# Optimization experiments

Hardware: AMD Instinct MI355X
Metric: run time of the kernel (lower is better)

The kernel has to match this reference:

```python
import jax, jax.numpy as jnp
import numpy as np

B, S, F, E, C = 8, 8192, 512, 128, 1000


def setup_inputs() -> dict:
    key = jax.random.key(0)
    k1, k2, k3, k4 = jax.random.split(key, 4)
    x = jax.random.normal(k1, (B, F), dtype=jnp.float32)
    support_x = jax.random.normal(k2, (B, S, F), dtype=jnp.float32)
    support_y = jax.random.uniform(k3, (B, S, C), dtype=jnp.float32)
    # xavier_uniform on (1, F, E): gain * sqrt(6/(fan_in+fan_out))
    limit = float(np.sqrt(6.0 / (F + E)))
    proj_weight = jax.random.uniform(k4, (1, F, E), dtype=jnp.float32,
                                     minval=-limit, maxval=limit)
    return {"x": x, "support_x": support_x, "support_y": support_y,
            "proj_weight": proj_weight}


def reference(x, support_x, support_y, proj_weight):
    W = proj_weight[0]  # (F, E); bmm with repeated weight == shared matmul
    xq = x @ W                               # (B, E) query embedding
    sx = jnp.einsum('bsf,fe->bse', support_x, W)  # (B, S, E)
    # euclidean kernel: scores = -||xq - sx||_2, shape (B, S)
    diff = xq[:, None, :] - sx               # (B, S, E)
    scores = -jnp.sqrt(jnp.sum(diff * diff, axis=-1))
    probs = jax.nn.softmax(scores, axis=-1)  # (B, S)
    out = jnp.einsum('bs,bsc->bc', probs, support_y)  # (B, C)
    return out
```

## Files before the change

kernel.cpp:

```cpp
#include <hip/hip_runtime.h>
#include <hip/hip_bf16.h>

#define BB 8
#define SS 8192
#define FF 512
#define EE 128
#define CC 1000

typedef __bf16 bf16x8 __attribute__((ext_vector_type(8)));
typedef float  f32x4  __attribute__((ext_vector_type(4)));

__global__ void k0_wt(const float* __restrict__ W, __bf16* __restrict__ Wt) {
    int idx = blockIdx.x * 256 + threadIdx.x;
    int e = idx & (EE - 1);
    int f = idx >> 7;
    Wt[e * FF + f] = (__bf16)W[f * EE + e];
}

__global__ __launch_bounds__(512, 4) void k_fused(
    const float* __restrict__ x,
    const float* __restrict__ sx,
    const __bf16* __restrict__ Wt,
    const float* __restrict__ y,
    float* __restrict__ pout,
    float* __restrict__ pden)
{
    __shared__ __bf16 lA[2][4][128][8];
    __shared__ __bf16 lB[2][4][128][8];
    __shared__ float  scp[2][128];
    __shared__ float  wv[128];

    const int tid   = threadIdx.x;
    const int b     = blockIdx.x >> 6;
    const int chunk = blockIdx.x & 63;
    const int srow0 = chunk << 7;
    const float* Xb = sx + ((size_t)b * SS + srow0) * FF;
    const float* xb = x + b * FF;

    const int rowS = tid >> 2;
    const int kq   = tid & 3;

    const int lane = tid & 63;
    const int w    = tid >> 6;
    const int wrow = (w >> 1) * 32;
    const int wcol = (w & 1) * 64;
    const int lg   = lane >> 4;
    const int lr   = lane & 15;

    f32x4 acc[2][4];
    #pragma unroll
    for (int m = 0; m < 2; m++)
        #pragma unroll
        for (int n = 0; n < 4; n++) { f32x4 z = {0.f, 0.f, 0.f, 0.f}; acc[m][n] = z; }

    float4 sReg[2], xReg[2];
    bf16x8 bReg;

    auto LOADT = [&](int t) {
        const float* pS = Xb + (size_t)rowS * FF + t * 32 + kq * 8;
        const float* pX = xb + t * 32 + kq * 8;
        #pragma unroll
        for (int i = 0; i < 2; i++) {
            sReg[i] = *(const float4*)(pS + 4 * i);
            xReg[i] = *(const float4*)(pX + 4 * i);
        }
        bReg = *(const bf16x8*)(Wt + (size_t)rowS * FF + t * 32 + kq * 8);
    };
    auto WRITET = [&](int buf) {
        __bf16 d[8];
        #pragma unroll
        for (int i = 0; i < 2; i++) {
            d[4*i+0] = (__bf16)(xReg[i].x - sReg[i].x);
            d[4*i+1] = (__bf16)(xReg[i].y - sReg[i].y);
            d[4*i+2] = (__bf16)(xReg[i].z - sReg[i].z);
            d[4*i+3] = (__bf16)(xReg[i].w - sReg[i].w);
        }
        *(bf16x8*)&lA[buf][kq][rowS][0] = *(bf16x8*)&d[0];
        *(bf16x8*)&lB[buf][kq][rowS][0] = bReg;
    };

    LOADT(0);
    WRITET(0);
    __syncthreads();

    for (int t = 0; t < 16; t++) {
        const int cur = t & 1;
        if (t < 15) LOADT(t + 1);
        bf16x8 af[2], bfr[4];
        #pragma unroll
        for (int m = 0; m < 2; m++)
            af[m] = *(const bf16x8*)&lA[cur][lg][wrow + m * 16 + lr][0];
        #pragma unroll
        for (int n = 0; n < 4; n++)
            bfr[n] = *(const bf16x8*)&lB[cur][lg][wcol + n * 16 + lr][0];
        #pragma unroll
        for (int m = 0; m < 2; m++)
            #pragma unroll
            for (int n = 0; n < 4; n++)
                acc[m][n] = __builtin_amdgcn_mfma_f32_16x16x32_bf16(af[m], bfr[n], acc[m][n], 0, 0, 0);
        if (t < 15) WRITET(cur ^ 1);
        __syncthreads();
    }

    float rp[2][4];
    #pragma unroll
    for (int m = 0; m < 2; m++)
        #pragma unroll
        for (int j = 0; j < 4; j++) {
            float s = 0.f;
            #pragma unroll
            for (int n = 0; n < 4; n++) { float v = acc[m][n][j]; s += v * v; }
            rp[m][j] = s;
        }
    #pragma unroll
    for (int mask = 1; mask < 16; mask <<= 1)
        #pragma unroll
        for (int m = 0; m < 2; m++)
            #pragma unroll
            for (int j = 0; j < 4; j++)
                rp[m][j] += __shfl_xor(rp[m][j], mask);

    if (lr == 0) {
        #pragma unroll
        for (int m = 0; m < 2; m++)
            #pragma unroll
            for (int j = 0; j < 4; j++)
                scp[w & 1][wrow + m * 16 + lg * 4 + j] = rp[m][j];
    }
    __syncthreads();
    if (tid < 128)
        wv[tid] = expf(-sqrtf(scp[0][tid] + scp[1][tid]));
    __syncthreads();

    if (w == 0) {
        float d = wv[lane] + wv[lane + 64];
        #pragma unroll
        for (int mask = 1; mask < 64; mask <<= 1)
            d += __shfl_xor(d, mask);
        if (lane == 0) pden[b * 64 + chunk] = d;
    }

    if (tid < 500) {
        float a0 = 0.f, a1 = 0.f;
        const float* base = y + ((size_t)b * SS + srow0) * CC + tid * 2;
        #pragma unroll 8
        for (int r = 0; r < 128; r++) {
            float2 v = *(const float2*)(base + (size_t)r * CC);
            float wgt = wv[r];
            a0 += wgt * v.x; a1 += wgt * v.y;
        }
        float2 res = {a0, a1};
        *(float2*)(pout + ((size_t)(b * 64 + chunk)) * CC + tid * 2) = res;
    }
}

__global__ void k4_final(const float* __restrict__ pout, const float* __restrict__ pden,
                         float* __restrict__ out) {
    int idx = blockIdx.x * 256 + threadIdx.x;
    if (idx >= BB * CC) return;
    int b = idx / CC, c = idx % CC;
    float den = 0.f;
    #pragma unroll 8
    for (int k = 0; k < 64; k++) den += pden[b * 64 + k];
    float num = 0.f;
    #pragma unroll 8
    for (int k = 0; k < 64; k++) num += pout[((size_t)(b * 64 + k)) * CC + c];
    out[idx] = num / den;
}

extern "C" void kernel_launch(void* const* d_in, const int* in_sizes, int n_in,
                              void* d_out, int out_size, void* d_ws, size_t ws_size,
                              hipStream_t stream) {
    const float* x  = (const float*)d_in[0];
    const float* sx = (const float*)d_in[1];
    const float* sy = (const float*)d_in[2];
    const float* W  = (const float*)d_in[3];

    char* ws = (char*)d_ws;
    __bf16* Wt   = (__bf16*)(ws);
    float*  pout = (float*)(ws + 131072);
    float*  pden = (float*)(ws + 131072 + 2048000);

    k0_wt<<<256, 256, 0, stream>>>(W, Wt);
    k_fused<<<512, 512, 0, stream>>>(x, sx, Wt, sy, pout, pden);
    k4_final<<<32, 256, 0, stream>>>(pout, pden, (float*)d_out);
}
```

Measured before the change: 92.87 us.

## Stage full W in LDS and stream A fragments directly from global to registers

Loads the entire bf16 transposed weight (128x512) into shared memory once, then has each wave own 16 rows and all 128 output columns. The A operand (x minus support row) is built directly in registers from global loads with a 3-deep software prefetch, which drops the per-step LDS staging and per-iteration __syncthreads. The cross-wave score reduction through shared memory also goes away. In exchange the kernel uses about 128KB of LDS and more registers (launch bounds lowered to 2 blocks), so occupancy falls and each wave does more MFMAs per k-step.

```diff
diff --git a/kernel.cpp b/kernel.cpp
--- a/kernel.cpp
+++ b/kernel.cpp
@@ -17,7 +17,7 @@
     Wt[e * FF + f] = (__bf16)W[f * EE + e];
 }
 
-__global__ __launch_bounds__(512, 4) void k_fused(
+__global__ __launch_bounds__(512, 2) void k_fused(
     const float* __restrict__ x,
     const float* __restrict__ sx,
     const __bf16* __restrict__ Wt,
@@ -25,119 +25,98 @@
     float* __restrict__ pout,
     float* __restrict__ pden)
 {
-    __shared__ __bf16 lA[2][4][128][8];
-    __shared__ __bf16 lB[2][4][128][8];
-    __shared__ float  scp[2][128];
+    __shared__ __bf16 lB[16][4][128][8];
     __shared__ float  wv[128];
 
     const int tid   = threadIdx.x;
     const int b     = blockIdx.x >> 6;
     const int chunk = blockIdx.x & 63;
     const int srow0 = chunk << 7;
-    const float* Xb = sx + ((size_t)b * SS + srow0) * FF;
-    const float* xb = x + b * FF;
-
-    const int rowS = tid >> 2;
-    const int kq   = tid & 3;
 
     const int lane = tid & 63;
     const int w    = tid >> 6;
-    const int wrow = (w >> 1) * 32;
-    const int wcol = (w & 1) * 64;
     const int lg   = lane >> 4;
     const int lr   = lane & 15;
 
-    f32x4 acc[2][4];
     #pragma unroll
-    for (int m = 0; m < 2; m++)
-        #pragma unroll
-        for (int n = 0; n < 4; n++) { f32x4 z = {0.f, 0.f, 0.f, 0.f}; acc[m][n] = z; }
+    for (int i = 0; i < 8; i++) {
+        int c  = tid + i * 512;
+        int e  = c >> 5;
+        int r  = c & 31;
+        int t  = r >> 1;
+        int kh = r & 1;
+        const __bf16* p = Wt + (size_t)e * FF + t * 32 + kh * 16;
+        *(bf16x8*)&lB[t][kh*2+0][e][0] = *(const bf16x8*)(p);
+        *(bf16x8*)&lB[t][kh*2+1][e][0] = *(const bf16x8*)(p + 8);
+    }
+    __syncthreads();
 
-    float4 sReg[2], xReg[2];
-    bf16x8 bReg;
+    const float* Ap = sx + ((size_t)b * SS + srow0 + w * 16 + lr) * FF + lg * 8;
+    const float* xp = x + b * FF + lg * 8;
 
-    auto LOADT = [&](int t) {
-        const float* pS = Xb + (size_t)rowS * FF + t * 32 + kq * 8;
-        const float* pX = xb + t * 32 + kq * 8;
-        #pragma unroll
-        for (int i = 0; i < 2; i++) {
-            sReg[i] = *(const float4*)(pS + 4 * i);
-            xReg[i] = *(const float4*)(pX + 4 * i);
-        }
-        bReg = *(const bf16x8*)(Wt + (size_t)rowS * FF + t * 32 + kq * 8);
+    f32x4 acc[8];
+    #pragma unroll
+    for (int n = 0; n < 8; n++) { f32x4 z = {0.f, 0.f, 0.f, 0.f}; acc[n] = z; }
+
+    float4 sS[4][2], xS[4][2];
+
+    auto LOAD = [&](int t, int slot) {
+        sS[slot][0] = *(const float4*)(Ap + t * 32);
+        sS[slot][1] = *(const float4*)(Ap + t * 32 + 4);
+        xS[slot][0] = *(const float4*)(xp + t * 32);
+        xS[slot][1] = *(const float4*)(xp + t * 32 + 4);
     };
-    auto WRITET = [&](int buf) {
+    auto COMPUTE = [&](int t, int slot) {
         __bf16 d[8];
         #pragma unroll
         for (int i = 0; i < 2; i++) {
-            d[4*i+0] = (__bf16)(xReg[i].x - sReg[i].x);
-            d[4*i+1] = (__bf16)(xReg[i].y - sReg[i].y);
-            d[4*i+2] = (__bf16)(xReg[i].z - sReg[i].z);
-            d[4*i+3] = (__bf16)(xReg[i].w - sReg[i].w);
+            d[4*i+0] = (__bf16)(xS[slot][i].x - sS[slot][i].x);
+            d[4*i+1] = (__bf16)(xS[slot][i].y - sS[slot][i].y);
+            d[4*i+2] = (__bf16)(xS[slot][i].z - sS[slot][i].z);
+            d[4*i+3] = (__bf16)(xS[slot][i].w - sS[slot][i].w);
         }
-        *(bf16x8*)&lA[buf][kq][rowS][0] = *(bf16x8*)&d[0];
-        *(bf16x8*)&lB[buf][kq][rowS][0] = bReg;
+        bf16x8 af = *(bf16x8*)d;
+        #pragma unroll
+        for (int n = 0; n < 8; n++) {
+            bf16x8 bfr = *(const bf16x8*)&lB[t][lg][n * 16 + lr][0];
+            acc[n] = __builtin_amdgcn_mfma_f32_16x16x32_bf16(af, bfr, acc[n], 0, 0, 0);
+        }
     };
 
-    LOADT(0);
-    WRITET(0);
-    __syncthreads();
-
+    LOAD(0, 0); LOAD(1, 1); LOAD(2, 2);
+    #pragma unroll
     for (int t = 0; t < 16; t++) {
-        const int cur = t & 1;
-        if (t < 15) LOADT(t + 1);
-        bf16x8 af[2], bfr[4];
-        #pragma unroll
-        for (int m = 0; m < 2; m++)
-            af[m] = *(const bf16x8*)&lA[cur][lg][wrow + m * 16 + lr][0];
-        #pragma unroll
-        for (int n = 0; n < 4; n++)
-            bfr[n] = *(const bf16x8*)&lB[cur][lg][wcol + n * 16 + lr][0];
-        #pragma unroll
-        for (int m = 0; m < 2; m++)
-            #pragma unroll
-            for (int n = 0; n < 4; n++)
-                acc[m][n] = __builtin_amdgcn_mfma_f32_16x16x32_bf16(af[m], bfr[n], acc[m][n], 0, 0, 0);
-        if (t < 15) WRITET(cur ^ 1);
-        __syncthreads();
+        COMPUTE(t, t & 3);
+        if (t + 3 < 16) LOAD(t + 3, (t + 3) & 3);
     }
 
-    float rp[2][4];
+    float rp[4];
     #pragma unroll
-    for (int m = 0; m < 2; m++)
+    for (int j = 0; j < 4; j++) {
+        float s = 0.f;
         #pragma unroll
-        for (int j = 0; j < 4; j++) {
-            float s = 0.f;
-            #pragma unroll
-            for (int n = 0; n < 4; n++) { float v = acc[m][n][j]; s += v * v; }
-            rp[m][j] = s;
-        }
+        for (int n = 0; n < 8; n++) { float v = acc[n][j]; s += v * v; }
+        rp[j] = s;
+    }
     #pragma unroll
     for (int mask = 1; mask < 16; mask <<= 1)
         #pragma unroll
-        for (int m = 0; m < 2; m++)
-            #pragma unroll
-            for (int j = 0; j < 4; j++)
-                rp[m][j] += __shfl_xor(rp[m][j], mask);
+        for (int j = 0; j < 4; j++)
+            rp[j] += __shfl_xor(rp[j], mask);
 
     if (lr == 0) {
         #pragma unroll
-        for (int m = 0; m < 2; m++)
-            #pragma unroll
-            for (int j = 0; j < 4; j++)
-                scp[w & 1][wrow + m * 16 + lg * 4 + j] = rp[m][j];
+        for (int j = 0; j < 4; j++)
+            wv[w * 16 + lg * 4 + j] = expf(-sqrtf(rp[j]));
     }
-    __syncthreads();
-    if (tid < 128)
-        wv[tid] = expf(-sqrtf(scp[0][tid] + scp[1][tid]));
     __syncthreads();
 
     if (w == 0) {
-        float d = wv[lane] + wv[lane + 64];
+        float dsum = wv[lane] + wv[lane + 64];
         #pragma unroll
         for (int mask = 1; mask < 64; mask <<= 1)
-            d += __shfl_xor(d, mask);
-        if (lane == 0) pden[b * 64 + chunk] = d;
+            dsum += __shfl_xor(dsum, mask);
+        if (lane == 0) pden[b * 64 + chunk] = dsum;
     }
 
     if (tid < 500) {
```

Result: slower. 97.93 us (+5.4%).
